# Kernel optimization log

Hardware: AMD Instinct MI355X
Metric: run time of the kernel (lower is better)

The kernel has to match this reference:

```python
import jax, jax.numpy as jnp
import numpy as np

B, S, D = 32, 8192, 128
SPARSITY = 0.5
CLUSTER = 4
HID = 256
MEM = 128
NCLS = 10
MASK_KEY = jax.random.key(1234)


def setup_inputs() -> dict:
    key = jax.random.key(0)
    ks = jax.random.split(key, 8)
    cin = CLUSTER * D  # 512
    return {
        "x": jax.random.normal(ks[0], (B, S, D), dtype=jnp.float32),
        "memory": jax.random.normal(ks[1], (B, MEM), dtype=jnp.float32),
        "W_fc": jax.random.normal(ks[2], (HID, cin), dtype=jnp.float32) / np.sqrt(cin),
        "b_fc": jax.random.normal(ks[3], (HID,), dtype=jnp.float32) * 0.01,
        "W_mem": jax.random.normal(ks[4], (MEM, HID), dtype=jnp.float32) / np.sqrt(HID),
        "b_mem": jax.random.normal(ks[5], (MEM,), dtype=jnp.float32) * 0.01,
        "W_out": jax.random.normal(ks[6], (NCLS, MEM), dtype=jnp.float32) / np.sqrt(MEM),
        "b_out": jax.random.normal(ks[7], (NCLS,), dtype=jnp.float32) * 0.01,
    }


def reference(x, memory, W_fc, b_fc, W_mem, b_mem, W_out, b_out):
    # --- SparseInformationExtraction: top-k tokens by L2 norm ---
    k = int(SPARSITY * S)  # 4096
    token_norms = jnp.linalg.norm(x, axis=-1)          # (B, S)
    _, topk_idx = jax.lax.top_k(token_norms, k)        # (B, k), sorted desc like torch.topk
    sparse_x = jnp.take_along_axis(x, topk_idx[:, :, None], axis=1)  # (B, k, D)

    # --- HierarchicalClustering: group CLUSTER tokens ---
    num_clusters = k // CLUSTER                        # 1024
    clustered = sparse_x.reshape(B, num_clusters, CLUSTER * D)  # (B, 1024, 512)

    # --- DynamicMaskingActivation: linear + bernoulli mask + relu ---
    h = jnp.einsum('bnc,hc->bnh', clustered, W_fc) + b_fc       # (B, 1024, HID)
    mask = jax.random.bernoulli(MASK_KEY, p=SPARSITY, shape=h.shape).astype(h.dtype)
    h = jax.nn.relu(h * mask)

    # --- SparseMemory: mean-pool + linear + residual relu ---
    x_compressed = jnp.mean(h, axis=1)                           # (B, HID)
    updated_memory = jax.nn.relu(x_compressed @ W_mem.T + b_mem + memory)  # (B, MEM)

    # --- output head ---
    output = updated_memory @ W_out.T + b_out                    # (B, NCLS)
    return (output, updated_memory)
```

## Files before the change

### kernel.cpp

```cpp
#include <hip/hip_runtime.h>
#include <stdint.h>

#define NB 32
#define NS 8192
#define ND 128
#define KTOP 4096
#define NCLUST 1024
#define CIN 512
#define HIDN 256
#define NMEM 128
#define NCLS 10
#define HALFCNT 4194304u

typedef unsigned long long ull;
typedef __attribute__((ext_vector_type(8))) short bf16x8;
typedef __attribute__((ext_vector_type(4))) float f32x4;

__device__ __forceinline__ unsigned int rotl32(unsigned int v, int r) {
  return (v << r) | (v >> (32 - r));
}

__device__ __forceinline__ void threefry_block(unsigned int& x0, unsigned int& x1) {
  const unsigned int k0 = 0u;
  const unsigned int k1 = 1234u;
  const unsigned int k2 = 0x1BD11BDAu ^ 0u ^ 1234u;
  x0 += k0; x1 += k1;
#define TF_R(r) { x0 += x1; x1 = rotl32(x1, (r)); x1 ^= x0; }
  TF_R(13) TF_R(15) TF_R(26) TF_R(6)   x0 += k1; x1 += k2 + 1u;
  TF_R(17) TF_R(29) TF_R(16) TF_R(24)  x0 += k2; x1 += k0 + 2u;
  TF_R(13) TF_R(15) TF_R(26) TF_R(6)   x0 += k0; x1 += k1 + 3u;
  TF_R(17) TF_R(29) TF_R(16) TF_R(24)  x0 += k1; x1 += k2 + 4u;
  TF_R(13) TF_R(15) TF_R(26) TF_R(6)   x0 += k2; x1 += k0 + 5u;
#undef TF_R
}

__device__ __forceinline__ bool mask_keep(unsigned int flat) {
  const bool low = flat < HALFCNT;
  unsigned int a, b;
  if (low) { a = flat;           b = flat + HALFCNT; }
  else     { a = flat - HALFCNT; b = flat; }
  threefry_block(a, b);
  const unsigned int w = low ? a : b;
  return (w & 0x80000000u) == 0u;
}

__device__ __forceinline__ unsigned int f2bf(float f) {
  unsigned int u = __float_as_uint(f);
  return (u + 0x7fffu + ((u >> 16) & 1u)) >> 16;
}
__device__ __forceinline__ unsigned int pack2bf(float lo, float hi) {
  return f2bf(lo) | (f2bf(hi) << 16);
}

__device__ __forceinline__ void gload_lds16(const void* g, void* l) {
  __builtin_amdgcn_global_load_lds(
      (const __attribute__((address_space(1))) unsigned int*)g,
      (__attribute__((address_space(3))) unsigned int*)l, 16, 0, 0);
}

__device__ __forceinline__ ull shfl_xor_u64(ull x, int m) {
  unsigned int lo = (unsigned int)x, hi = (unsigned int)(x >> 32);
  lo = (unsigned int)__shfl_xor((int)lo, m);
  hi = (unsigned int)__shfl_xor((int)hi, m);
  return ((ull)hi << 32) | lo;
}

#define NORM_BLOCKS 32768
__global__ __launch_bounds__(256) void norms_kernel(
    const float* __restrict__ x, ull* __restrict__ keys,
    float* __restrict__ xc, const float* __restrict__ Wfc,
    unsigned short* __restrict__ Wbf) {
  const int blk = blockIdx.x;
  if (blk >= NORM_BLOCKS) {
    const int t = (blk - NORM_BLOCKS) * 256 + threadIdx.x;
    const float4* s = (const float4*)(Wfc + (size_t)t * 8);
    const float4 a = s[0], b = s[1];
    uint4 o;
    o.x = pack2bf(a.x, a.y); o.y = pack2bf(a.z, a.w);
    o.z = pack2bf(b.x, b.y); o.w = pack2bf(b.z, b.w);
    *(uint4*)(Wbf + (size_t)t * 8) = o;
    return;
  }
  const int t = blk * 256 + threadIdx.x;
  if (t < NB * HIDN) xc[t] = 0.0f;
  const int token = t >> 5;
  const int l = t & 31;
  const float4 v = ((const float4*)(x + (size_t)token * ND))[l];
  float ss = v.x * v.x + v.y * v.y + v.z * v.z + v.w * v.w;
#pragma unroll
  for (int off = 16; off >= 1; off >>= 1) ss += __shfl_xor(ss, off);
  if (l == 0) {
    const float nrm = sqrtf(ss);
    const unsigned int ub = ~__float_as_uint(nrm);
    keys[token] = ((ull)ub << 32) | (unsigned int)(token & (NS - 1));
  }
}

#define CMPEX(J, K, HF)                                                 \
  {                                                                     \
    _Pragma("unroll") for (int r = 0; r < 8; ++r) {                     \
      if ((r & (J)) == 0) {                                             \
        const int i0 = (tid << 3) + r;                                  \
        const bool up2 = (((i0 & (K)) == 0) != (HF));                   \
        const ull lo = v[r], hi = v[r | (J)];                           \
        const ull mn = lo < hi ? lo : hi;                               \
        const ull mx = lo < hi ? hi : lo;                               \
        v[r] = up2 ? mn : mx;                                           \
        v[r | (J)] = up2 ? mx : mn;                                     \
      }                                                                 \
    }                                                                   \
  }

__global__ __launch_bounds__(512) void sortA_kernel(ull* __restrict__ keys) {
  __shared__ ull slds[8 * 512];
  const int b = blockIdx.x >> 1;
  const int half = blockIdx.x & 1;
  const bool hf = (half != 0);
  const int tid = threadIdx.x;
  ull v[8];
  ull* base = keys + (size_t)b * NS + half * 4096;
#pragma unroll
  for (int r = 0; r < 8; ++r) v[r] = base[tid * 8 + r];

  for (int k = 2; k <= 4096; k <<= 1) {
    for (int j = k >> 1; j >= 512; j >>= 1) {
      __syncthreads();
#pragma unroll
      for (int r = 0; r < 8; ++r) slds[r * 512 + tid] = v[r];
      __syncthreads();
      const int ptid = tid ^ (j >> 3);
      const bool up2 = ((((tid << 3) & k) == 0) != hf);
      const bool lower = (((tid << 3) & j) == 0);
      const bool keepmin = (up2 == lower);
#pragma unroll
      for (int r = 0; r < 8; ++r) {
        const ull p = slds[r * 512 + ptid];
        const ull mn = v[r] < p ? v[r] : p;
        const ull mx = v[r] < p ? p : v[r];
        v[r] = keepmin ? mn : mx;
      }
    }
    {
      const int jstart = (k >> 1) < 256 ? (k >> 1) : 256;
      for (int j = jstart; j >= 8; j >>= 1) {
        const int lanemask = j >> 3;
        const bool up2 = ((((tid << 3) & k) == 0) != hf);
        const bool lower = (((tid << 3) & j) == 0);
        const bool keepmin = (up2 == lower);
#pragma unroll
        for (int r = 0; r < 8; ++r) {
          const ull p = shfl_xor_u64(v[r], lanemask);
          const ull mn = v[r] < p ? v[r] : p;
          const ull mx = v[r] < p ? p : v[r];
          v[r] = keepmin ? mn : mx;
        }
      }
    }
    if (k >= 8)      { CMPEX(4, k, hf) CMPEX(2, k, hf) CMPEX(1, k, hf) }
    else if (k == 4) { CMPEX(2, k, hf) CMPEX(1, k, hf) }
    else             { CMPEX(1, k, hf) }
  }

#pragma unroll
  for (int r = 0; r < 8; ++r) base[tid * 8 + r] = v[r];
}

__global__ __launch_bounds__(512) void sortB_kernel(
    const ull* __restrict__ keys, unsigned int* __restrict__ topk) {
  __shared__ ull slds[8 * 512];
  const int b = blockIdx.x;
  const int tid = threadIdx.x;
  ull v[8];
  const ull* base = keys + (size_t)b * NS;
#pragma unroll
  for (int r = 0; r < 8; ++r) v[r] = base[tid * 8 + r];
#pragma unroll
  for (int r = 0; r < 8; ++r) {
    const ull u = base[4096 + tid * 8 + r];
    v[r] = v[r] < u ? v[r] : u;
  }
  for (int j = 2048; j >= 512; j >>= 1) {
    __syncthreads();
#pragma unroll
    for (int r = 0; r < 8; ++r) slds[r * 512 + tid] = v[r];
    __syncthreads();
    const int ptid = tid ^ (j >> 3);
    const bool keepmin = (((tid << 3) & j) == 0);
#pragma unroll
    for (int r = 0; r < 8; ++r) {
      const ull p = slds[r * 512 + ptid];
      const ull mn = v[r] < p ? v[r] : p;
      const ull mx = v[r] < p ? p : v[r];
      v[r] = keepmin ? mn : mx;
    }
  }
  for (int j = 256; j >= 8; j >>= 1) {
    const int lanemask = j >> 3;
    const bool keepmin = (((tid << 3) & j) == 0);
#pragma unroll
    for (int r = 0; r < 8; ++r) {
      const ull p = shfl_xor_u64(v[r], lanemask);
      const ull mn = v[r] < p ? v[r] : p;
      const ull mx = v[r] < p ? p : v[r];
      v[r] = keepmin ? mn : mx;
    }
  }
  CMPEX(4, 8192, false) CMPEX(2, 8192, false) CMPEX(1, 8192, false)
#pragma unroll
  for (int r = 0; r < 8; ++r)
    topk[b * KTOP + tid * 8 + r] = (unsigned int)v[r];
}

__global__ __launch_bounds__(512) void gemm_kernel(
    const float* __restrict__ x, const unsigned short* __restrict__ Wbf,
    const float* __restrict__ bfc, const unsigned int* __restrict__ topk,
    float* __restrict__ xc) {
  __shared__ __align__(16) unsigned short Al[128 * 64];
  __shared__ __align__(16) unsigned short Bl[256 * 64];
  __shared__ int tokL[512];
  __shared__ float red[8][64];

  const int bid = blockIdx.x;
  const int bb = bid >> 3;
  const int m0 = (bid & 7) * 128;
  const int t = threadIdx.x;
  const int w = t >> 6, l = t & 63;
  const int wr = w >> 2, wc = w & 3;
  const int lrow = l & 15, lk = l >> 4;

  tokL[t] = (int)topk[bb * KTOP + m0 * 4 + t];
  __syncthreads();

  f32x4 acc[4][4];
#pragma unroll
  for (int m = 0; m < 4; ++m)
#pragma unroll
    for (int n = 0; n < 4; ++n) acc[m][n] = (f32x4)0.f;

  const int arow = t >> 2, aseg = t & 3;
  float4 ar[4];
  {
    const int cs = aseg;
    const int token = tokL[arow * 4 + (cs >> 3)];
    const float* asrc = x + ((size_t)bb * NS + token) * ND + ((cs * 16) & 127);
#pragma unroll
    for (int q = 0; q < 4; ++q) ar[q] = ((const float4*)asrc)[q];
  }

  const int brow_in8 = l >> 3;
  const int bkb_src = ((l & 7) * 16) ^ (brow_in8 << 4);

  for (int kt = 0; kt < 8; ++kt) {
    {
      uint4 p0, p1;
      p0.x = pack2bf(ar[0].x, ar[0].y); p0.y = pack2bf(ar[0].z, ar[0].w);
      p0.z = pack2bf(ar[1].x, ar[1].y); p0.w = pack2bf(ar[1].z, ar[1].w);
      p1.x = pack2bf(ar[2].x, ar[2].y); p1.y = pack2bf(ar[2].z, ar[2].w);
      p1.z = pack2bf(ar[3].x, ar[3].y); p1.w = pack2bf(ar[3].z, ar[3].w);
      const int swz = (arow & 7) << 4;
      const int base = arow * 128;
      *(uint4*)((char*)Al + base + ((aseg * 32) ^ swz)) = p0;
      *(uint4*)((char*)Al + base + ((aseg * 32 + 16) ^ swz)) = p1;
    }
    {
#pragma unroll
      for (int q = 0; q < 4; ++q) {
        const int grp = q * 8 + w;
        const int row = grp * 8 + brow_in8;
        const char* g = (const char*)Wbf + (size_t)row * 1024 + kt * 128 +
                        bkb_src;
        gload_lds16(g, (char*)Bl + grp * 1024);
      }
    }
    __syncthreads();

    if (kt < 7) {
      const int cs = (kt + 1) * 4 + aseg;
      const int token = tokL[arow * 4 + (cs >> 3)];
      const float* asrc = x + ((size_t)bb * NS + token) * ND + ((cs * 16) & 127);
#pragma unroll
      for (int q = 0; q < 4; ++q) ar[q] = ((const float4*)asrc)[q];
    }

    const int swz = (lrow & 7) << 4;
#pragma unroll
    for (int kk = 0; kk < 2; ++kk) {
      const int koff = (kk * 64 + lk * 16) ^ swz;
      bf16x8 af[4], bfr[4];
#pragma unroll
      for (int m = 0; m < 4; ++m)
        af[m] = *(const bf16x8*)((const char*)Al +
                                 (wr * 64 + m * 16 + lrow) * 128 + koff);
#pragma unroll
      for (int n = 0; n < 4; ++n)
        bfr[n] = *(const bf16x8*)((const char*)Bl +
                                  (wc * 64 + n * 16 + lrow) * 128 + koff);
#pragma unroll
      for (int m = 0; m < 4; ++m)
#pragma unroll
        for (int n = 0; n < 4; ++n)
          acc[m][n] = __builtin_amdgcn_mfma_f32_16x16x32_bf16(
              af[m], bfr[n], acc[m][n], 0, 0, 0);
    }
    __syncthreads();
  }

  float bias_n[4];
#pragma unroll
  for (int n = 0; n < 4; ++n) bias_n[n] = bfc[wc * 64 + n * 16 + lrow];

  const int rowbase = m0 + wr * 64 + lk * 4;
  float csum[4] = {0.f, 0.f, 0.f, 0.f};
#pragma unroll
  for (int n = 0; n < 4; ++n) {
    const unsigned int gcol = (unsigned int)(wc * 64 + n * 16 + lrow);
#pragma unroll
    for (int m = 0; m < 4; ++m) {
#pragma unroll
      for (int reg = 0; reg < 4; ++reg) {
        const unsigned int gm =
            (unsigned int)(bb * NCLUST + rowbase + m * 16 + reg);
        const unsigned int flat = gm * 256u + gcol;
        const bool keep = mask_keep(flat);
        float vv = acc[m][n][reg] + bias_n[n];
        vv = keep ? fmaxf(vv, 0.0f) : 0.0f;
        csum[n] += vv;
      }
    }
  }
#pragma unroll
  for (int n = 0; n < 4; ++n) {
    csum[n] += __shfl_xor(csum[n], 16);
    csum[n] += __shfl_xor(csum[n], 32);
  }
  if (l < 16) {
#pragma unroll
    for (int n = 0; n < 4; ++n) red[w][n * 16 + l] = csum[n];
  }
  __syncthreads();
  if (t < HIDN) {
    const int cwc = t >> 6, c = t & 63;
    const float s = red[cwc][c] + red[cwc + 4][c];
    atomicAdd(&xc[bb * HIDN + t], s);
  }
}

__global__ __launch_bounds__(128) void tail_kernel(
    const float* __restrict__ xc, const float* __restrict__ memory,
    const float* __restrict__ Wmem, const float* __restrict__ bmem,
    const float* __restrict__ Wout, const float* __restrict__ bout,
    float* __restrict__ out) {
  __shared__ __align__(16) float xl[HIDN];
  __shared__ float ul[NMEM];
  const int b = blockIdx.x, t = threadIdx.x;
  xl[t]       = xc[b * HIDN + t] * (1.0f / NCLUST);
  xl[t + 128] = xc[b * HIDN + t + 128] * (1.0f / NCLUST);
  __syncthreads();
  float a = 0.0f;
  const float4* wr2 = (const float4*)(Wmem + (size_t)t * HIDN);
#pragma unroll 4
  for (int q = 0; q < HIDN / 4; ++q) {
    const float4 wv = wr2[q];
    const float4 xv = *(const float4*)&xl[q * 4];
    a = fmaf(wv.x, xv.x, a); a = fmaf(wv.y, xv.y, a);
    a = fmaf(wv.z, xv.z, a); a = fmaf(wv.w, xv.w, a);
  }
  a += bmem[t] + memory[b * NMEM + t];
  a = fmaxf(a, 0.0f);
  ul[t] = a;
  out[NB * NCLS + b * NMEM + t] = a;
  __syncthreads();
  if (t < NCLS) {
    float o = 0.0f;
#pragma unroll 4
    for (int m = 0; m < NMEM; ++m) o = fmaf(ul[m], Wout[t * NMEM + m], o);
    out[b * NCLS + t] = o + bout[t];
  }
}

extern "C" void kernel_launch(void* const* d_in, const int* in_sizes, int n_in,
                              void* d_out, int out_size, void* d_ws, size_t ws_size,
                              hipStream_t stream) {
  (void)in_sizes; (void)n_in; (void)out_size; (void)ws_size;
  const float* x    = (const float*)d_in[0];
  const float* mem  = (const float*)d_in[1];
  const float* Wfc  = (const float*)d_in[2];
  const float* bfc  = (const float*)d_in[3];
  const float* Wmem = (const float*)d_in[4];
  const float* bmem = (const float*)d_in[5];
  const float* Wout = (const float*)d_in[6];
  const float* bout = (const float*)d_in[7];
  float* out = (float*)d_out;

  char* ws = (char*)d_ws;
  ull* keys = (ull*)ws;
  unsigned int* topk = (unsigned int*)(ws + (size_t)NB * NS * 8);
  float* xc = (float*)(ws + (size_t)NB * NS * 8 + (size_t)NB * KTOP * 4);
  unsigned short* Wbf = (unsigned short*)(ws + (size_t)NB * NS * 8 +
                                          (size_t)NB * KTOP * 4 +
                                          (size_t)NB * HIDN * 4);

  norms_kernel<<<dim3(NORM_BLOCKS + 64), 256, 0, stream>>>(x, keys, xc, Wfc,
                                                           Wbf);
  sortA_kernel<<<dim3(NB * 2), 512, 0, stream>>>(keys);
  sortB_kernel<<<dim3(NB), 512, 0, stream>>>(keys, topk);
  gemm_kernel<<<dim3(256), 512, 0, stream>>>(x, Wbf, bfc, topk, xc);
  tail_kernel<<<dim3(NB), 128, 0, stream>>>(xc, mem, Wmem, bmem, Wout, bout, out);
}
```

Before: 277.0 us.

## Pair batches b and b+16 per tile to share one threefry call for both mask bits

The GEMM kernel is re-tiled so each block handles 16 clusters from batch b and the same 16 clusters from batch b+16. The flat mask indices of these two rows differ by exactly half the count, so a single threefry block yields both mask words, halving RNG work in the epilogue. Blocks become smaller (256 threads, 32 rows) and there are 1024 of them, which adds occupancy but reloads the full W tile per block. The LDS reduction is replaced by direct atomics, so more atomic traffic goes to xc.

```diff
diff --git a/kernel.cpp b/kernel.cpp
--- a/kernel.cpp
+++ b/kernel.cpp
@@ -32,16 +32,6 @@
   TF_R(17) TF_R(29) TF_R(16) TF_R(24)  x0 += k1; x1 += k2 + 4u;
   TF_R(13) TF_R(15) TF_R(26) TF_R(6)   x0 += k2; x1 += k0 + 5u;
 #undef TF_R
-}
-
-__device__ __forceinline__ bool mask_keep(unsigned int flat) {
-  const bool low = flat < HALFCNT;
-  unsigned int a, b;
-  if (low) { a = flat;           b = flat + HALFCNT; }
-  else     { a = flat - HALFCNT; b = flat; }
-  threefry_block(a, b);
-  const unsigned int w = low ? a : b;
-  return (w & 0x80000000u) == 0u;
 }
 
 __device__ __forceinline__ unsigned int f2bf(float f) {
@@ -211,40 +201,44 @@
     topk[b * KTOP + tid * 8 + r] = (unsigned int)v[r];
 }
 
-__global__ __launch_bounds__(512) void gemm_kernel(
+__global__ __launch_bounds__(256, 4) void gemm_kernel(
     const float* __restrict__ x, const unsigned short* __restrict__ Wbf,
     const float* __restrict__ bfc, const unsigned int* __restrict__ topk,
     float* __restrict__ xc) {
-  __shared__ __align__(16) unsigned short Al[128 * 64];
+  __shared__ __align__(16) unsigned short Al[32 * 64];
   __shared__ __align__(16) unsigned short Bl[256 * 64];
-  __shared__ int tokL[512];
-  __shared__ float red[8][64];
+  __shared__ int tokL[128];
 
   const int bid = blockIdx.x;
-  const int bb = bid >> 3;
-  const int m0 = (bid & 7) * 128;
+  const int bb = bid >> 6;
+  const int m0c = (bid & 63) * 16;
   const int t = threadIdx.x;
   const int w = t >> 6, l = t & 63;
-  const int wr = w >> 2, wc = w & 3;
   const int lrow = l & 15, lk = l >> 4;
 
-  tokL[t] = (int)topk[bb * KTOP + m0 * 4 + t];
+  if (t < 128) {
+    const int r = t >> 2, s = t & 3;
+    const int batch = (r < 16) ? bb : bb + 16;
+    tokL[t] = (int)topk[batch * KTOP + (m0c + (r & 15)) * 4 + s];
+  }
   __syncthreads();
 
-  f32x4 acc[4][4];
-#pragma unroll
-  for (int m = 0; m < 4; ++m)
+  f32x4 acc[2][4];
+#pragma unroll
+  for (int m = 0; m < 2; ++m)
 #pragma unroll
     for (int n = 0; n < 4; ++n) acc[m][n] = (f32x4)0.f;
 
-  const int arow = t >> 2, aseg = t & 3;
-  float4 ar[4];
+  const int arow = t >> 3, kq = t & 7;
+  const int abatch = (arow < 16) ? bb : bb + 16;
+  float4 ar[2];
   {
-    const int cs = aseg;
-    const int token = tokL[arow * 4 + (cs >> 3)];
-    const float* asrc = x + ((size_t)bb * NS + token) * ND + ((cs * 16) & 127);
-#pragma unroll
-    for (int q = 0; q < 4; ++q) ar[q] = ((const float4*)asrc)[q];
+    const int cs = kq;
+    const int token = tokL[arow * 4 + (cs >> 4)];
+    const float* asrc =
+        x + ((size_t)abatch * NS + token) * ND + (cs & 15) * 8;
+    ar[0] = ((const float4*)asrc)[0];
+    ar[1] = ((const float4*)asrc)[1];
   }
 
   const int brow_in8 = l >> 3;
@@ -252,20 +246,16 @@
 
   for (int kt = 0; kt < 8; ++kt) {
     {
-      uint4 p0, p1;
+      uint4 p0;
       p0.x = pack2bf(ar[0].x, ar[0].y); p0.y = pack2bf(ar[0].z, ar[0].w);
       p0.z = pack2bf(ar[1].x, ar[1].y); p0.w = pack2bf(ar[1].z, ar[1].w);
-      p1.x = pack2bf(ar[2].x, ar[2].y); p1.y = pack2bf(ar[2].z, ar[2].w);
-      p1.z = pack2bf(ar[3].x, ar[3].y); p1.w = pack2bf(ar[3].z, ar[3].w);
       const int swz = (arow & 7) << 4;
-      const int base = arow * 128;
-      *(uint4*)((char*)Al + base + ((aseg * 32) ^ swz)) = p0;
-      *(uint4*)((char*)Al + base + ((aseg * 32 + 16) ^ swz)) = p1;
+      *(uint4*)((char*)Al + arow * 128 + ((kq * 16) ^ swz)) = p0;
     }
     {
 #pragma unroll
-      for (int q = 0; q < 4; ++q) {
-        const int grp = q * 8 + w;
+      for (int q = 0; q < 8; ++q) {
+        const int grp = w * 8 + q;
         const int row = grp * 8 + brow_in8;
         const char* g = (const char*)Wbf + (size_t)row * 1024 + kt * 128 +
                         bkb_src;
@@ -275,28 +265,29 @@
     __syncthreads();
 
     if (kt < 7) {
-      const int cs = (kt + 1) * 4 + aseg;
-      const int token = tokL[arow * 4 + (cs >> 3)];
-      const float* asrc = x + ((size_t)bb * NS + token) * ND + ((cs * 16) & 127);
-#pragma unroll
-      for (int q = 0; q < 4; ++q) ar[q] = ((const float4*)asrc)[q];
+      const int cs = (kt + 1) * 8 + kq;
+      const int token = tokL[arow * 4 + (cs >> 4)];
+      const float* asrc =
+          x + ((size_t)abatch * NS + token) * ND + (cs & 15) * 8;
+      ar[0] = ((const float4*)asrc)[0];
+      ar[1] = ((const float4*)asrc)[1];
     }
 
     const int swz = (lrow & 7) << 4;
 #pragma unroll
     for (int kk = 0; kk < 2; ++kk) {
       const int koff = (kk * 64 + lk * 16) ^ swz;
-      bf16x8 af[4], bfr[4];
-#pragma unroll
-      for (int m = 0; m < 4; ++m)
+      bf16x8 af[2], bfr[4];
+#pragma unroll
+      for (int m = 0; m < 2; ++m)
         af[m] = *(const bf16x8*)((const char*)Al +
-                                 (wr * 64 + m * 16 + lrow) * 128 + koff);
+                                 (m * 16 + lrow) * 128 + koff);
 #pragma unroll
       for (int n = 0; n < 4; ++n)
         bfr[n] = *(const bf16x8*)((const char*)Bl +
-                                  (wc * 64 + n * 16 + lrow) * 128 + koff);
-#pragma unroll
-      for (int m = 0; m < 4; ++m)
+                                  (w * 64 + n * 16 + lrow) * 128 + koff);
+#pragma unroll
+      for (int m = 0; m < 2; ++m)
 #pragma unroll
         for (int n = 0; n < 4; ++n)
           acc[m][n] = __builtin_amdgcn_mfma_f32_16x16x32_bf16(
@@ -307,41 +298,41 @@
 
   float bias_n[4];
 #pragma unroll
-  for (int n = 0; n < 4; ++n) bias_n[n] = bfc[wc * 64 + n * 16 + lrow];
-
-  const int rowbase = m0 + wr * 64 + lk * 4;
-  float csum[4] = {0.f, 0.f, 0.f, 0.f};
+  for (int n = 0; n < 4; ++n) bias_n[n] = bfc[w * 64 + n * 16 + lrow];
+
+  float csum[2][4] = {{0.f, 0.f, 0.f, 0.f}, {0.f, 0.f, 0.f, 0.f}};
 #pragma unroll
   for (int n = 0; n < 4; ++n) {
-    const unsigned int gcol = (unsigned int)(wc * 64 + n * 16 + lrow);
-#pragma unroll
-    for (int m = 0; m < 4; ++m) {
-#pragma unroll
-      for (int reg = 0; reg < 4; ++reg) {
-        const unsigned int gm =
-            (unsigned int)(bb * NCLUST + rowbase + m * 16 + reg);
-        const unsigned int flat = gm * 256u + gcol;
-        const bool keep = mask_keep(flat);
-        float vv = acc[m][n][reg] + bias_n[n];
-        vv = keep ? fmaxf(vv, 0.0f) : 0.0f;
-        csum[n] += vv;
-      }
-    }
-  }
-#pragma unroll
-  for (int n = 0; n < 4; ++n) {
-    csum[n] += __shfl_xor(csum[n], 16);
-    csum[n] += __shfl_xor(csum[n], 32);
-  }
+    const unsigned int gcol = (unsigned int)(w * 64 + n * 16 + lrow);
+#pragma unroll
+    for (int reg = 0; reg < 4; ++reg) {
+      const unsigned int crow = (unsigned int)(m0c + lk * 4 + reg);
+      const unsigned int flat = ((unsigned int)bb * 1024u + crow) * 256u + gcol;
+      unsigned int a = flat, b2 = flat + HALFCNT;
+      threefry_block(a, b2);
+      const bool keep0 = (a & 0x80000000u) == 0u;
+      const bool keep1 = (b2 & 0x80000000u) == 0u;
+      float v0 = acc[0][n][reg] + bias_n[n];
+      float v1 = acc[1][n][reg] + bias_n[n];
+      v0 = keep0 ? fmaxf(v0, 0.0f) : 0.0f;
+      v1 = keep1 ? fmaxf(v1, 0.0f) : 0.0f;
+      csum[0][n] += v0;
+      csum[1][n] += v1;
+    }
+  }
+#pragma unroll
+  for (int p = 0; p < 2; ++p)
+#pragma unroll
+    for (int n = 0; n < 4; ++n) {
+      csum[p][n] += __shfl_xor(csum[p][n], 16);
+      csum[p][n] += __shfl_xor(csum[p][n], 32);
+    }
   if (l < 16) {
 #pragma unroll
-    for (int n = 0; n < 4; ++n) red[w][n * 16 + l] = csum[n];
-  }
-  __syncthreads();
-  if (t < HIDN) {
-    const int cwc = t >> 6, c = t & 63;
-    const float s = red[cwc][c] + red[cwc + 4][c];
-    atomicAdd(&xc[bb * HIDN + t], s);
+    for (int n = 0; n < 4; ++n) {
+      atomicAdd(&xc[bb * HIDN + w * 64 + n * 16 + l], csum[0][n]);
+      atomicAdd(&xc[(bb + 16) * HIDN + w * 64 + n * 16 + l], csum[1][n]);
+    }
   }
 }
 
@@ -404,6 +395,6 @@
                                                            Wbf);
   sortA_kernel<<<dim3(NB * 2), 512, 0, stream>>>(keys);
   sortB_kernel<<<dim3(NB), 512, 0, stream>>>(keys, topk);
-  gemm_kernel<<<dim3(256), 512, 0, stream>>>(x, Wbf, bfc, topk, xc);
+  gemm_kernel<<<dim3(1024), 256, 0, stream>>>(x, Wbf, bfc, topk, xc);
   tail_kernel<<<dim3(NB), 128, 0, stream>>>(xc, mem, Wmem, bmem, Wout, bout, out);
 }
```

Result: faster. 269.8 us (-2.6%).
